# Kernel tuning notes

Hardware: AMD Instinct MI355X
Metric: run time of the kernel (lower is better)

## Reference

```python
import jax, jax.numpy as jnp
import numpy as np

B, C_IN, L = 4, 128, 2048
HEADS, C_HEAD = 8, 32
HIDDEN = HEADS * C_HEAD  # 256
EPS = 1e-5


def setup_inputs() -> dict:
    key = jax.random.key(0)
    ks = jax.random.split(key, 6)
    return {
        "x": jax.random.normal(ks[0], (B, C_IN, L), dtype=jnp.float32),
        "w_qkv": jax.random.normal(ks[1], (3 * HIDDEN, C_IN), dtype=jnp.float32) * 0.05,
        "b_qkv": jax.random.normal(ks[2], (3 * HIDDEN,), dtype=jnp.float32) * 0.05,
        "w_out": jax.random.normal(ks[3], (C_IN, HIDDEN), dtype=jnp.float32) * 0.05,
        "b_out": jax.random.normal(ks[4], (C_IN,), dtype=jnp.float32) * 0.05,
        "bn_weight": jnp.ones((C_IN,), dtype=jnp.float32),
        "bn_bias": jnp.zeros((C_IN,), dtype=jnp.float32),
        "bn_mean": jnp.zeros((C_IN,), dtype=jnp.float32),
        "bn_var": jnp.ones((C_IN,), dtype=jnp.float32),
    }


def reference(x, w_qkv, b_qkv, w_out, b_out, bn_weight, bn_bias, bn_mean, bn_var):
    # 1x1 conv == channel matmul: (B, 3*hidden, L)
    qkv = jnp.einsum('oi,bil->bol', w_qkv, x) + b_qkv[None, :, None]
    # '(qkv heads c) l -> qkv heads l c' (batched)
    qkv = qkv.reshape(B, 3, HEADS, C_HEAD, L).transpose(1, 0, 2, 4, 3)  # (3,B,H,L,c)
    q, k, v = qkv[0], qkv[1], qkv[2]
    # Faithful quirk: original scales q by sqrt(q.shape[1]) == sqrt(L), not sqrt(c)
    q = q / jnp.sqrt(jnp.float32(L))
    # scores (B,H,L,L), softmax over last axis
    scores = jnp.einsum('bhqd,bhkd->bhqk', q, k)
    ctx = jax.nn.softmax(scores, axis=-1)
    # Faithful quirk: 'hca,hcb->hab' contracts over the QUERY axis of ctx
    attn = jnp.einsum('bhqa,bhqd->bhad', ctx, v)  # (B,H,L,c)
    # 'heads l h -> (heads h) l'
    attn = attn.transpose(0, 1, 3, 2).reshape(B, HIDDEN, L)
    out = jnp.einsum('oi,bil->bol', w_out, attn) + b_out[None, :, None]
    out = out + x
    # BatchNorm inference mode with running stats, per-channel
    inv = bn_weight / jnp.sqrt(bn_var + EPS)
    out = out * inv[None, :, None] + (bn_bias - bn_mean * inv)[None, :, None]
    return out
```

## Files before the change

### kernel.cpp

```cpp
#include <hip/hip_runtime.h>
#include <math.h>

#define BB 4
#define CIN 128
#define LL 2048
#define HH 8
#define CH 32
#define HID 256

typedef __attribute__((ext_vector_type(8))) __bf16 bf16x8;
typedef __attribute__((ext_vector_type(4))) float f32x4;
typedef __attribute__((ext_vector_type(16))) float f32x16;

static __device__ __forceinline__ unsigned int f2bf(float f) {
    union { __bf16 b; unsigned short s; } u;
    u.b = (__bf16)f;
    return (unsigned int)u.s;
}
static __device__ __forceinline__ float bf2f(unsigned int s) {
    union { float f; unsigned int u; } x;
    x.u = s << 16;
    return x.f;
}

#define MFMA   __builtin_amdgcn_mfma_f32_16x16x32_bf16
#define MFMA32 __builtin_amdgcn_mfma_f32_32x32x16_bf16
#define E2(x)  __builtin_amdgcn_exp2f(x)

__global__ __launch_bounds__(256) void prep_kernel(
        const float* __restrict__ x, const float* __restrict__ w,
        const float* __restrict__ wo,
        unsigned short* __restrict__ xb, unsigned short* __restrict__ wb,
        unsigned short* __restrict__ wob) {
    __shared__ float tr2[128][65];
    const int t = threadIdx.x;
    const int bid = blockIdx.x;
    if (bid >= 224) {
        const int idx = ((bid - 224) * 256 + t) * 4;
        float4 v = *(const float4*)(wo + idx);
        uint2 o;
        o.x = f2bf(v.x) | (f2bf(v.y) << 16);
        o.y = f2bf(v.z) | (f2bf(v.w) << 16);
        *(uint2*)(wob + idx) = o;
        return;
    }
    if (bid >= 128) {
        const int idx = ((bid - 128) * 256 + t) * 4;
        float4 v = *(const float4*)(w + idx);
        uint2 o;
        o.x = f2bf(v.x) | (f2bf(v.y) << 16);
        o.y = f2bf(v.z) | (f2bf(v.w) << 16);
        *(uint2*)(wb + idx) = o;
        return;
    }
    const int lt = bid & 31, b = bid >> 5;
    const int l0 = lt * 64;
    const int ll = t & 63, ig = t >> 6;
    const float* xp = x + (size_t)b * CIN * LL + l0 + ll;
    #pragma unroll
    for (int k = 0; k < 32; ++k) {
        const int i = k * 4 + ig;
        tr2[i][ll] = xp[(size_t)i * LL];
    }
    __syncthreads();
    const int l = t >> 2, i0 = (t & 3) * 32;
    unsigned short* dst = xb + ((size_t)b * LL + l0 + l) * CIN + i0;
    unsigned int wv[16];
    #pragma unroll
    for (int j = 0; j < 16; ++j)
        wv[j] = f2bf(tr2[i0 + 2*j][l]) | (f2bf(tr2[i0 + 2*j + 1][l]) << 16);
    *(uint4*)(dst)      = make_uint4(wv[0],  wv[1],  wv[2],  wv[3]);
    *(uint4*)(dst + 8)  = make_uint4(wv[4],  wv[5],  wv[6],  wv[7]);
    *(uint4*)(dst + 16) = make_uint4(wv[8],  wv[9],  wv[10], wv[11]);
    *(uint4*)(dst + 24) = make_uint4(wv[12], wv[13], wv[14], wv[15]);
}

__global__ __launch_bounds__(256) void qkv_mfma(
        const unsigned short* __restrict__ xb, const unsigned short* __restrict__ wb,
        const float* __restrict__ b_qkv,
        unsigned short* __restrict__ qb, unsigned short* __restrict__ kb,
        unsigned short* __restrict__ vtb) {
    __shared__ unsigned short xlds[64][136];
    __shared__ unsigned short wlds2[32][136];
    __shared__ float tr[32 * 65];
    const int t = threadIdx.x, w = t >> 6, lane = t & 63;
    const int r = lane & 15, gq = lane >> 4;
    const int lt = blockIdx.x;
    const int g  = blockIdx.y;
    const int b  = blockIdx.z;
    const int sel = g >> 3, h = g & 7;
    const int obase = sel * 256 + h * 32;
    const int l0 = lt * 64;

    {
        const unsigned short* xsrc = xb + ((size_t)b * LL + l0) * CIN;
        #pragma unroll
        for (int k2 = 0; k2 < 4; ++k2) {
            int idx = t + k2 * 256;
            int row = idx >> 4, col8 = (idx & 15) * 8;
            *(uint4*)&xlds[row][col8] = *(const uint4*)(xsrc + row * CIN + col8);
        }
        const unsigned short* wsrc = wb + (size_t)obase * CIN;
        #pragma unroll
        for (int k2 = 0; k2 < 2; ++k2) {
            int idx = t + k2 * 256;
            int row = idx >> 4, col8 = (idx & 15) * 8;
            *(uint4*)&wlds2[row][col8] = *(const uint4*)(wsrc + row * CIN + col8);
        }
    }
    __syncthreads();

    f32x4 acc0 = {0,0,0,0}, acc1 = {0,0,0,0};
    #pragma unroll
    for (int ks = 0; ks < 4; ++ks) {
        bf16x8 bfr = *(const bf16x8*)&xlds[w * 16 + r][gq * 8 + ks * 32];
        bf16x8 a0  = *(const bf16x8*)&wlds2[r][gq * 8 + ks * 32];
        bf16x8 a1  = *(const bf16x8*)&wlds2[16 + r][gq * 8 + ks * 32];
        acc0 = MFMA(a0, bfr, acc0, 0, 0, 0);
        acc1 = MFMA(a1, bfr, acc1, 0, 0, 0);
    }
    const float scale = (sel == 0) ? 0.03187935835f : 1.0f;
    #pragma unroll
    for (int reg = 0; reg < 4; ++reg) {
        const int oc0 = gq * 4 + reg;
        tr[oc0 * 65 + w * 16 + r] = (acc0[reg] + b_qkv[obase + oc0]) * scale;
        const int oc1 = 16 + gq * 4 + reg;
        tr[oc1 * 65 + w * 16 + r] = (acc1[reg] + b_qkv[obase + oc1]) * scale;
    }
    __syncthreads();

    if (sel == 2) {
        unsigned short* dst = vtb + ((size_t)(b * HH + h) * CH) * LL + l0;
        #pragma unroll
        for (int rr = 0; rr < 8; ++rr) {
            int flat = rr * 256 + t;
            int c = flat >> 6, l = flat & 63;
            dst[(size_t)c * LL + l] = (unsigned short)f2bf(tr[c * 65 + l]);
        }
    } else {
        unsigned short* dst = (sel == 0 ? qb : kb)
                              + ((size_t)(b * HH + h) * LL + l0) * CH;
        #pragma unroll
        for (int rr = 0; rr < 8; ++rr) {
            int flat = rr * 256 + t;
            int c = flat & 31, lr = flat >> 5;
            dst[flat] = (unsigned short)f2bf(tr[c * 65 + lr]);
        }
    }
}

__global__ __launch_bounds__(512, 4) void denom_mfma(
        const unsigned short* __restrict__ qb,
        const unsigned short* __restrict__ kb,
        unsigned short* __restrict__ vtb) {
    __shared__ unsigned short klds[2][64][40];
    __shared__ float zz[128];
    const int t = threadIdx.x, wave = t >> 6, lane = t & 63;
    const int id = blockIdx.x;
    const int bh = (id & 7) * 4 + (id >> 7);
    const int qt = (id >> 3) & 15;
    const int r = lane & 15, g = lane >> 4;
    const int q0 = qt * 128 + wave * 16;

    bf16x8 afrag = *(const bf16x8*)(qb + ((size_t)bh * LL + q0 + r) * CH + 8 * g);

    const int si = t;
    const unsigned short* ksrc = kb + (size_t)bh * LL * CH + si * 8;
    const int sdst = (si >> 2) * 40 + (si & 3) * 8;

    float z0 = 0.f, z1 = 0.f, z2 = 0.f, z3 = 0.f;
    const f32x4 zero = {0.f, 0.f, 0.f, 0.f};

    if (t < 256) {
        uint4 sreg = *(const uint4*)(ksrc);
        *(uint4*)(&klds[0][0][0] + sdst) = sreg;
    }
    __syncthreads();

    const int rb = r * 40 + 8 * g;
    for (int c = 0; c < 32; ++c) {
        const int cur = c & 1;
        uint4 nreg;
        if (c < 31 && t < 256)
            nreg = *(const uint4*)(ksrc + (size_t)(c + 1) * 2048);
        const unsigned short* kc = &klds[cur][0][0];
        #pragma unroll
        for (int s = 0; s < 4; ++s) {
            bf16x8 bf = *(const bf16x8*)(kc + s * 16 * 40 + rb);
            f32x4 d = MFMA(afrag, bf, zero, 0, 0, 0);
            z0 += E2(d[0]); z1 += E2(d[1]); z2 += E2(d[2]); z3 += E2(d[3]);
        }
        __syncthreads();
        if (c < 31 && t < 256)
            *(uint4*)(&klds[cur ^ 1][0][0] + sdst) = nreg;
        __syncthreads();
    }

    #pragma unroll
    for (int m = 1; m < 16; m <<= 1) {
        z0 += __shfl_xor(z0, m); z1 += __shfl_xor(z1, m);
        z2 += __shfl_xor(z2, m); z3 += __shfl_xor(z3, m);
    }
    if (r == 0)
        *(float4*)&zz[wave * 16 + 4 * g] = make_float4(z0, z1, z2, z3);
    __syncthreads();
    if (t < 128) zz[t] = 1.0f / zz[t];
    __syncthreads();

    const int d = t >> 4, qo = (t & 15) * 8;
    unsigned short* vrow = vtb + ((size_t)bh * CH + d) * LL + qt * 128 + qo;
    uint4 v = *(const uint4*)vrow;
    const float* zp = &zz[qo];
    unsigned int w0, w1, w2, w3;
    w0 = f2bf(bf2f(v.x & 0xFFFFu) * zp[0]) | (f2bf(bf2f(v.x >> 16) * zp[1]) << 16);
    w1 = f2bf(bf2f(v.y & 0xFFFFu) * zp[2]) | (f2bf(bf2f(v.y >> 16) * zp[3]) << 16);
    w2 = f2bf(bf2f(v.z & 0xFFFFu) * zp[4]) | (f2bf(bf2f(v.z >> 16) * zp[5]) << 16);
    w3 = f2bf(bf2f(v.w & 0xFFFFu) * zp[6]) | (f2bf(bf2f(v.w >> 16) * zp[7]) << 16);
    *(uint4*)vrow = make_uint4(w0, w1, w2, w3);
}

__global__ __launch_bounds__(512, 4) void attn_mfma(
        const unsigned short* __restrict__ qb,
        const unsigned short* __restrict__ kb,
        const unsigned short* __restrict__ vtb,
        float* __restrict__ attnT) {
    __shared__ unsigned short qlds[2][32][40];
    __shared__ unsigned short vlds[2][32][40];
    const int t = threadIdx.x, wave = t >> 6, lane = t & 63;
    const int ln = lane & 31, hi = lane >> 5;
    const int id = blockIdx.x;
    const int bhqh = (id & 7) * 8 + (id >> 6);
    const int at = (id >> 3) & 7;
    const int bh = bhqh >> 1, qh = bhqh & 1;
    const int b = bh >> 3, h = bh & 7;
    const int a0 = at * 256 + wave * 32;
    const int q00 = qh * 1024;

    const unsigned short* kp = kb + ((size_t)bh * LL + a0 + ln) * CH + 8 * hi;
    const bf16x8 kf0 = *(const bf16x8*)kp;
    const bf16x8 kf1 = *(const bf16x8*)(kp + 16);

    const int si = t & 127;
    const unsigned short* qsrc = qb + ((size_t)bh * LL + q00) * CH + si * 8;
    const unsigned short* vsrc = vtb + ((size_t)bh * CH + (si >> 2)) * LL
                                 + q00 + (si & 3) * 8;
    const int sdst = (si >> 2) * 40 + (si & 3) * 8;
    unsigned short* const ql0 = &qlds[0][0][0];
    unsigned short* const ql1 = &qlds[1][0][0];
    unsigned short* const vl0 = &vlds[0][0][0];
    unsigned short* const vl1 = &vlds[1][0][0];

    f32x16 acc = {0.f,0.f,0.f,0.f,0.f,0.f,0.f,0.f,0.f,0.f,0.f,0.f,0.f,0.f,0.f,0.f};
    const f32x16 zero16 = {0.f,0.f,0.f,0.f,0.f,0.f,0.f,0.f,0.f,0.f,0.f,0.f,0.f,0.f,0.f,0.f};

#define CVTPK(dst, lo_, hi_) \
    asm("v_cvt_pk_bf16_f32 %0, %1, %2" : "=v"(dst) : "v"(lo_), "v"(hi_))
#define SWAPH(a_, b_) \
    asm("v_permlane32_swap_b32 %0, %1" : "+v"(a_), "+v"(b_))

    {
        uint4 sreg;
        if (wave < 2)      sreg = *(const uint4*)(qsrc);
        else if (wave < 4) sreg = *(const uint4*)(vsrc);
        if (wave < 2)      *(uint4*)(ql0 + sdst) = sreg;
        else if (wave < 4) *(uint4*)(vl0 + sdst) = sreg;
    }
    __syncthreads();

    const int rdq = ln * 40 + 8 * hi;
    #pragma unroll 2
    for (int n = 0; n < 32; ++n) {
        const int cur = n & 1;
        uint4 nreg;
        if (n < 31) {
            if (wave < 2)      nreg = *(const uint4*)(qsrc + (n + 1) * 1024);
            else if (wave < 4) nreg = *(const uint4*)(vsrc + (n + 1) * 32);
        }
        const unsigned short* qc = cur ? ql1 : ql0;
        const unsigned short* vc = cur ? vl1 : vl0;
        bf16x8 qa0 = *(const bf16x8*)(qc + rdq);
        bf16x8 qa1 = *(const bf16x8*)(qc + rdq + 16);
        bf16x8 vb0 = *(const bf16x8*)(vc + rdq);
        bf16x8 vb1 = *(const bf16x8*)(vc + rdq + 16);
        f32x16 s = MFMA32(qa0, kf0, zero16, 0, 0, 0);
        s = MFMA32(qa1, kf1, s, 0, 0, 0);
        unsigned int w0, w1, w2, w3, w4, w5, w6, w7;
        {
            float p0  = E2(s[0]),  p1  = E2(s[1]),  p2  = E2(s[2]),  p3  = E2(s[3]);
            float p4  = E2(s[4]),  p5  = E2(s[5]),  p6  = E2(s[6]),  p7  = E2(s[7]);
            float p8  = E2(s[8]),  p9  = E2(s[9]),  p10 = E2(s[10]), p11 = E2(s[11]);
            float p12 = E2(s[12]), p13 = E2(s[13]), p14 = E2(s[14]), p15 = E2(s[15]);
            CVTPK(w0, p0,  p1);  CVTPK(w1, p2,  p3);
            CVTPK(w2, p4,  p5);  CVTPK(w3, p6,  p7);
            CVTPK(w4, p8,  p9);  CVTPK(w5, p10, p11);
            CVTPK(w6, p12, p13); CVTPK(w7, p14, p15);
            SWAPH(w0, w2); SWAPH(w1, w3); SWAPH(w4, w6); SWAPH(w5, w7);
        }
        union { uint4 u; bf16x8 v; } pa0, pa1;
        pa0.u = make_uint4(w0, w1, w2, w3);
        pa1.u = make_uint4(w4, w5, w6, w7);
        __builtin_amdgcn_s_setprio(1);
        acc = MFMA32(pa0.v, vb0, acc, 0, 0, 0);
        acc = MFMA32(pa1.v, vb1, acc, 0, 0, 0);
        __builtin_amdgcn_s_setprio(0);
        __syncthreads();
        if (n < 31) {
            unsigned short* qd = cur ? ql0 : ql1;
            unsigned short* vd = cur ? vl0 : vl1;
            if (wave < 2)      *(uint4*)(qd + sdst) = nreg;
            else if (wave < 4) *(uint4*)(vd + sdst) = nreg;
        }
        __syncthreads();
    }

#undef SWAPH
#undef CVTPK

    float* ob = attnT + ((size_t)qh * BB * HID + (size_t)b * HID + h * CH + ln) * LL
                + a0 + 4 * hi;
    *(f32x4*)(ob +  0) = __builtin_shufflevector(acc, acc,  0,  1,  2,  3);
    *(f32x4*)(ob +  8) = __builtin_shufflevector(acc, acc,  4,  5,  6,  7);
    *(f32x4*)(ob + 16) = __builtin_shufflevector(acc, acc,  8,  9, 10, 11);
    *(f32x4*)(ob + 24) = __builtin_shufflevector(acc, acc, 12, 13, 14, 15);
}

__global__ __launch_bounds__(256, 4) void out_mfma(
        const float* __restrict__ attnT, const unsigned short* __restrict__ wob,
        const float* __restrict__ x, const float* __restrict__ b_out,
        const float* __restrict__ bnw, const float* __restrict__ bnb,
        const float* __restrict__ bnm, const float* __restrict__ bnv,
        float* __restrict__ out) {
    __shared__ unsigned short alds[2][32][40];
    __shared__ unsigned short wlds[2][128][40];
    const int t = threadIdx.x, wave = t >> 6, lane = t & 63;
    const int ln = lane & 31, hi = lane >> 5;
    const int id = blockIdx.x;
    const int bid = (id & 7) * 32 + (id >> 3);
    const int b = bid >> 6, lt = bid & 63;
    const int l0 = lt * 32;
    const size_t PART = (size_t)BB * HID * LL;

    const int si = t >> 3, sl4 = (t & 7) * 4;
    const float* ap0 = attnT + ((size_t)b * HID + si) * LL + l0 + sl4;
    const unsigned short* wsrc0 = wob + (size_t)(t >> 2) * HID + (t & 3) * 8;
    const unsigned short* wsrc1 = wsrc0 + (size_t)64 * HID;
    unsigned short* const wdst0 = &wlds[0][t >> 2][(t & 3) * 8];
    const int WBUF = 128 * 40;

    f32x16 acc = {0.f,0.f,0.f,0.f,0.f,0.f,0.f,0.f,0.f,0.f,0.f,0.f,0.f,0.f,0.f,0.f};

    {
        f32x4 a0 = *(const f32x4*)(ap0);
        f32x4 a1 = *(const f32x4*)(ap0 + PART);
        uint4 w0 = *(const uint4*)(wsrc0);
        uint4 w1 = *(const uint4*)(wsrc1);
        #pragma unroll
        for (int j = 0; j < 4; ++j)
            alds[0][sl4 + j][si] = (unsigned short)f2bf(a0[j] + a1[j]);
        *(uint4*)(wdst0) = w0;
        *(uint4*)(wdst0 + 64 * 40) = w1;
    }
    __syncthreads();

    for (int c = 0; c < 8; ++c) {
        const int cur = c & 1;
        f32x4 na0, na1; uint4 nw0, nw1;
        if (c < 7) {
            na0 = *(const f32x4*)(ap0 + (size_t)(c + 1) * 32 * LL);
            na1 = *(const f32x4*)(ap0 + (size_t)(c + 1) * 32 * LL + PART);
            nw0 = *(const uint4*)(wsrc0 + (c + 1) * 32);
            nw1 = *(const uint4*)(wsrc1 + (c + 1) * 32);
        }
        const unsigned short* wc = &wlds[cur][0][0] + (wave * 32 + ln) * 40 + 8 * hi;
        const unsigned short* ac = &alds[cur][0][0] + ln * 40 + 8 * hi;
        bf16x8 af0 = *(const bf16x8*)(wc);
        bf16x8 af1 = *(const bf16x8*)(wc + 16);
        bf16x8 bf0 = *(const bf16x8*)(ac);
        bf16x8 bf1 = *(const bf16x8*)(ac + 16);
        acc = MFMA32(af0, bf0, acc, 0, 0, 0);
        acc = MFMA32(af1, bf1, acc, 0, 0, 0);
        __syncthreads();
        if (c < 7) {
            const int nb = cur ^ 1;
            #pragma unroll
            for (int j = 0; j < 4; ++j)
                alds[nb][sl4 + j][si] = (unsigned short)f2bf(na0[j] + na1[j]);
            *(uint4*)(wdst0 + nb * 2 * WBUF / 2) = nw0;
            *(uint4*)(wdst0 + nb * 2 * WBUF / 2 + 64 * 40) = nw1;
        }
        __syncthreads();
    }

    #pragma unroll
    for (int reg = 0; reg < 16; ++reg) {
        const int o = wave * 32 + (reg & 3) + 8 * (reg >> 2) + 4 * hi;
        const float inv = bnw[o] / sqrtf(bnv[o] + 1e-5f);
        const float sh  = bnb[o] - bnm[o] * inv;
        const size_t idx = ((size_t)b * CIN + o) * LL + l0 + ln;
        float val = acc[reg] + b_out[o] + x[idx];
        out[idx] = val * inv + sh;
    }
}

extern "C" void kernel_launch(void* const* d_in, const int* in_sizes, int n_in,
                              void* d_out, int out_size, void* d_ws, size_t ws_size,
                              hipStream_t stream) {
    const float* x      = (const float*)d_in[0];
    const float* w_qkv  = (const float*)d_in[1];
    const float* b_qkv  = (const float*)d_in[2];
    const float* w_out  = (const float*)d_in[3];
    const float* b_out  = (const float*)d_in[4];
    const float* bnw    = (const float*)d_in[5];
    const float* bnb    = (const float*)d_in[6];
    const float* bnm    = (const float*)d_in[7];
    const float* bnv    = (const float*)d_in[8];
    float* out = (float*)d_out;

    const size_t NBH = (size_t)BB * HH;
    const size_t QKV_ELEMS = NBH * LL * CH;
    unsigned short* qb    = (unsigned short*)d_ws;
    unsigned short* kb    = qb + QKV_ELEMS;
    unsigned short* vtb   = kb + QKV_ELEMS;
    float* attnT = (float*)(vtb + QKV_ELEMS);
    unsigned short* xb  = (unsigned short*)(attnT + 2 * (size_t)BB * HID * LL);
    unsigned short* wb  = xb + (size_t)BB * LL * CIN;
    unsigned short* wob = wb + (size_t)3 * HID * CIN;

    prep_kernel<<<dim3(256), 256, 0, stream>>>(x, w_qkv, w_out, xb, wb, wob);
    qkv_mfma<<<dim3(32, 24, BB), 256, 0, stream>>>(xb, wb, b_qkv, qb, kb, vtb);
    denom_mfma<<<dim3(512), 512, 0, stream>>>(qb, kb, vtb);
    attn_mfma<<<dim3(512), 512, 0, stream>>>(qb, kb, vtb, attnT);
    out_mfma<<<dim3(256), 256, 0, stream>>>(attnT, wob, x, b_out,
                                            bnw, bnb, bnm, bnv, out);
}
```

Measured before the change: 75.46 us.

## Double LDS stage size and drop redundant barrier per double-buffered iteration

In the denominator and attention kernels, each loop iteration now stages twice as many K (or Q/V) rows in LDS. This halves the trip count and spreads the staging loads over all 512 threads instead of half of them. In all three MFMA kernels the barrier before writing the next buffer is removed, since double buffering means the write goes to the other buffer. The goal is to cut barrier and loop overhead and use all waves for global loads. The cost is more LDS per block, which may reduce occupancy.

```diff
diff --git a/kernel.cpp b/kernel.cpp
--- a/kernel.cpp
+++ b/kernel.cpp
@@ -153,7 +153,7 @@
         const unsigned short* __restrict__ qb,
         const unsigned short* __restrict__ kb,
         unsigned short* __restrict__ vtb) {
-    __shared__ unsigned short klds[2][64][40];
+    __shared__ unsigned short klds[2][128][40];
     __shared__ float zz[128];
     const int t = threadIdx.x, wave = t >> 6, lane = t & 63;
     const int id = blockIdx.x;
@@ -164,34 +164,29 @@
 
     bf16x8 afrag = *(const bf16x8*)(qb + ((size_t)bh * LL + q0 + r) * CH + 8 * g);
 
-    const int si = t;
-    const unsigned short* ksrc = kb + (size_t)bh * LL * CH + si * 8;
-    const int sdst = (si >> 2) * 40 + (si & 3) * 8;
+    const unsigned short* ksrc = kb + ((size_t)bh * LL + (t >> 2)) * CH + (t & 3) * 8;
+    const int sdst = (t >> 2) * 40 + (t & 3) * 8;
 
     float z0 = 0.f, z1 = 0.f, z2 = 0.f, z3 = 0.f;
     const f32x4 zero = {0.f, 0.f, 0.f, 0.f};
 
-    if (t < 256) {
-        uint4 sreg = *(const uint4*)(ksrc);
-        *(uint4*)(&klds[0][0][0] + sdst) = sreg;
-    }
+    *(uint4*)(&klds[0][0][0] + sdst) = *(const uint4*)(ksrc);
     __syncthreads();
 
     const int rb = r * 40 + 8 * g;
-    for (int c = 0; c < 32; ++c) {
+    for (int c = 0; c < 16; ++c) {
         const int cur = c & 1;
         uint4 nreg;
-        if (c < 31 && t < 256)
-            nreg = *(const uint4*)(ksrc + (size_t)(c + 1) * 2048);
+        if (c < 15)
+            nreg = *(const uint4*)(ksrc + (size_t)(c + 1) * 4096);
         const unsigned short* kc = &klds[cur][0][0];
         #pragma unroll
-        for (int s = 0; s < 4; ++s) {
+        for (int s = 0; s < 8; ++s) {
             bf16x8 bf = *(const bf16x8*)(kc + s * 16 * 40 + rb);
             f32x4 d = MFMA(afrag, bf, zero, 0, 0, 0);
             z0 += E2(d[0]); z1 += E2(d[1]); z2 += E2(d[2]); z3 += E2(d[3]);
         }
-        __syncthreads();
-        if (c < 31 && t < 256)
+        if (c < 15)
             *(uint4*)(&klds[cur ^ 1][0][0] + sdst) = nreg;
         __syncthreads();
     }
@@ -224,8 +219,8 @@
         const unsigned short* __restrict__ kb,
         const unsigned short* __restrict__ vtb,
         float* __restrict__ attnT) {
-    __shared__ unsigned short qlds[2][32][40];
-    __shared__ unsigned short vlds[2][32][40];
+    __shared__ unsigned short qlds[2][64][40];
+    __shared__ unsigned short vlds[2][64][40];
     const int t = threadIdx.x, wave = t >> 6, lane = t & 63;
     const int ln = lane & 31, hi = lane >> 5;
     const int id = blockIdx.x;
@@ -240,11 +235,14 @@
     const bf16x8 kf0 = *(const bf16x8*)kp;
     const bf16x8 kf1 = *(const bf16x8*)(kp + 16);
 
-    const int si = t & 127;
-    const unsigned short* qsrc = qb + ((size_t)bh * LL + q00) * CH + si * 8;
-    const unsigned short* vsrc = vtb + ((size_t)bh * CH + (si >> 2)) * LL
-                                 + q00 + (si & 3) * 8;
-    const int sdst = (si >> 2) * 40 + (si & 3) * 8;
+    const int ts = t & 255;
+    const unsigned short* qsrc = qb + ((size_t)bh * LL + q00 + (ts >> 2)) * CH
+                                 + (ts & 3) * 8;
+    const int vsub = ts >> 7, vd = (ts >> 2) & 31, vq = (ts & 3) * 8;
+    const unsigned short* vsrc = vtb + ((size_t)bh * CH + vd) * LL + q00
+                                 + vsub * 32 + vq;
+    const int sdstq = (ts >> 2) * 40 + (ts & 3) * 8;
+    const int sdstv = (vsub * 32 + vd) * 40 + vq;
     unsigned short* const ql0 = &qlds[0][0][0];
     unsigned short* const ql1 = &qlds[1][0][0];
     unsigned short* const vl0 = &vlds[0][0][0];
@@ -258,57 +256,51 @@
 #define SWAPH(a_, b_) \
     asm("v_permlane32_swap_b32 %0, %1" : "+v"(a_), "+v"(b_))
 
-    {
-        uint4 sreg;
-        if (wave < 2)      sreg = *(const uint4*)(qsrc);
-        else if (wave < 4) sreg = *(const uint4*)(vsrc);
-        if (wave < 2)      *(uint4*)(ql0 + sdst) = sreg;
-        else if (wave < 4) *(uint4*)(vl0 + sdst) = sreg;
-    }
-    __syncthreads();
-
-    const int rdq = ln * 40 + 8 * hi;
-    #pragma unroll 2
-    for (int n = 0; n < 32; ++n) {
+    if (wave < 4) *(uint4*)(ql0 + sdstq) = *(const uint4*)(qsrc);
+    else          *(uint4*)(vl0 + sdstv) = *(const uint4*)(vsrc);
+    __syncthreads();
+
+    for (int n = 0; n < 16; ++n) {
         const int cur = n & 1;
         uint4 nreg;
-        if (n < 31) {
-            if (wave < 2)      nreg = *(const uint4*)(qsrc + (n + 1) * 1024);
-            else if (wave < 4) nreg = *(const uint4*)(vsrc + (n + 1) * 32);
+        if (n < 15) {
+            if (wave < 4) nreg = *(const uint4*)(qsrc + (size_t)(n + 1) * 2048);
+            else          nreg = *(const uint4*)(vsrc + (n + 1) * 64);
         }
         const unsigned short* qc = cur ? ql1 : ql0;
         const unsigned short* vc = cur ? vl1 : vl0;
-        bf16x8 qa0 = *(const bf16x8*)(qc + rdq);
-        bf16x8 qa1 = *(const bf16x8*)(qc + rdq + 16);
-        bf16x8 vb0 = *(const bf16x8*)(vc + rdq);
-        bf16x8 vb1 = *(const bf16x8*)(vc + rdq + 16);
-        f32x16 s = MFMA32(qa0, kf0, zero16, 0, 0, 0);
-        s = MFMA32(qa1, kf1, s, 0, 0, 0);
-        unsigned int w0, w1, w2, w3, w4, w5, w6, w7;
-        {
-            float p0  = E2(s[0]),  p1  = E2(s[1]),  p2  = E2(s[2]),  p3  = E2(s[3]);
-            float p4  = E2(s[4]),  p5  = E2(s[5]),  p6  = E2(s[6]),  p7  = E2(s[7]);
-            float p8  = E2(s[8]),  p9  = E2(s[9]),  p10 = E2(s[10]), p11 = E2(s[11]);
-            float p12 = E2(s[12]), p13 = E2(s[13]), p14 = E2(s[14]), p15 = E2(s[15]);
-            CVTPK(w0, p0,  p1);  CVTPK(w1, p2,  p3);
-            CVTPK(w2, p4,  p5);  CVTPK(w3, p6,  p7);
-            CVTPK(w4, p8,  p9);  CVTPK(w5, p10, p11);
-            CVTPK(w6, p12, p13); CVTPK(w7, p14, p15);
-            SWAPH(w0, w2); SWAPH(w1, w3); SWAPH(w4, w6); SWAPH(w5, w7);
-        }
-        union { uint4 u; bf16x8 v; } pa0, pa1;
-        pa0.u = make_uint4(w0, w1, w2, w3);
-        pa1.u = make_uint4(w4, w5, w6, w7);
-        __builtin_amdgcn_s_setprio(1);
-        acc = MFMA32(pa0.v, vb0, acc, 0, 0, 0);
-        acc = MFMA32(pa1.v, vb1, acc, 0, 0, 0);
-        __builtin_amdgcn_s_setprio(0);
-        __syncthreads();
-        if (n < 31) {
-            unsigned short* qd = cur ? ql0 : ql1;
-            unsigned short* vd = cur ? vl0 : vl1;
-            if (wave < 2)      *(uint4*)(qd + sdst) = nreg;
-            else if (wave < 4) *(uint4*)(vd + sdst) = nreg;
+        #pragma unroll
+        for (int s2 = 0; s2 < 2; ++s2) {
+            const int rdq = (s2 * 32 + ln) * 40 + 8 * hi;
+            bf16x8 qa0 = *(const bf16x8*)(qc + rdq);
+            bf16x8 qa1 = *(const bf16x8*)(qc + rdq + 16);
+            bf16x8 vb0 = *(const bf16x8*)(vc + rdq);
+            bf16x8 vb1 = *(const bf16x8*)(vc + rdq + 16);
+            f32x16 s = MFMA32(qa0, kf0, zero16, 0, 0, 0);
+            s = MFMA32(qa1, kf1, s, 0, 0, 0);
+            unsigned int w0, w1, w2, w3, w4, w5, w6, w7;
+            {
+                float p0  = E2(s[0]),  p1  = E2(s[1]),  p2  = E2(s[2]),  p3  = E2(s[3]);
+                float p4  = E2(s[4]),  p5  = E2(s[5]),  p6  = E2(s[6]),  p7  = E2(s[7]);
+                float p8  = E2(s[8]),  p9  = E2(s[9]),  p10 = E2(s[10]), p11 = E2(s[11]);
+                float p12 = E2(s[12]), p13 = E2(s[13]), p14 = E2(s[14]), p15 = E2(s[15]);
+                CVTPK(w0, p0,  p1);  CVTPK(w1, p2,  p3);
+                CVTPK(w2, p4,  p5);  CVTPK(w3, p6,  p7);
+                CVTPK(w4, p8,  p9);  CVTPK(w5, p10, p11);
+                CVTPK(w6, p12, p13); CVTPK(w7, p14, p15);
+                SWAPH(w0, w2); SWAPH(w1, w3); SWAPH(w4, w6); SWAPH(w5, w7);
+            }
+            union { uint4 u; bf16x8 v; } pa0, pa1;
+            pa0.u = make_uint4(w0, w1, w2, w3);
+            pa1.u = make_uint4(w4, w5, w6, w7);
+            __builtin_amdgcn_s_setprio(1);
+            acc = MFMA32(pa0.v, vb0, acc, 0, 0, 0);
+            acc = MFMA32(pa1.v, vb1, acc, 0, 0, 0);
+            __builtin_amdgcn_s_setprio(0);
+        }
+        if (n < 15) {
+            if (wave < 4) *(uint4*)((cur ? ql0 : ql1) + sdstq) = nreg;
+            else          *(uint4*)((cur ? vl0 : vl1) + sdstv) = nreg;
         }
         __syncthreads();
     }
@@ -339,13 +331,13 @@
     const int b = bid >> 6, lt = bid & 63;
     const int l0 = lt * 32;
     const size_t PART = (size_t)BB * HID * LL;
+    const int WBUF = 128 * 40;
 
     const int si = t >> 3, sl4 = (t & 7) * 4;
     const float* ap0 = attnT + ((size_t)b * HID + si) * LL + l0 + sl4;
     const unsigned short* wsrc0 = wob + (size_t)(t >> 2) * HID + (t & 3) * 8;
     const unsigned short* wsrc1 = wsrc0 + (size_t)64 * HID;
     unsigned short* const wdst0 = &wlds[0][t >> 2][(t & 3) * 8];
-    const int WBUF = 128 * 40;
 
     f32x16 acc = {0.f,0.f,0.f,0.f,0.f,0.f,0.f,0.f,0.f,0.f,0.f,0.f,0.f,0.f,0.f,0.f};
 
@@ -379,14 +371,13 @@
         bf16x8 bf1 = *(const bf16x8*)(ac + 16);
         acc = MFMA32(af0, bf0, acc, 0, 0, 0);
         acc = MFMA32(af1, bf1, acc, 0, 0, 0);
-        __syncthreads();
         if (c < 7) {
             const int nb = cur ^ 1;
             #pragma unroll
             for (int j = 0; j < 4; ++j)
                 alds[nb][sl4 + j][si] = (unsigned short)f2bf(na0[j] + na1[j]);
-            *(uint4*)(wdst0 + nb * 2 * WBUF / 2) = nw0;
-            *(uint4*)(wdst0 + nb * 2 * WBUF / 2 + 64 * 40) = nw1;
+            *(uint4*)(wdst0 + nb * WBUF) = nw0;
+            *(uint4*)(wdst0 + nb * WBUF + 64 * 40) = nw1;
         }
         __syncthreads();
     }
```

New measurement: 71.18 us. 1.06x faster.
